# Performance work log

Measured on AMD Instinct MI355X. Metric: run time of the kernel, lower is better.

Reference implementation:

```python
import jax, jax.numpy as jnp
import numpy as np

B, D, NNZ = 64, 8192, 1024      # batch, data_dim, nonzeros per row (exact)
DE, DQK = 256, 256              # id_embed_dim, qk_dim


def setup_inputs() -> dict:
    key = jax.random.key(0)
    k_pos, k_val, k_e, k_wq, k_bq, k_wk, k_bk = jax.random.split(key, 7)
    # x: [B, D] with exactly NNZ nonzero entries per row
    pos = jax.random.uniform(k_pos, (B, D)).argsort(axis=1)[:, :NNZ]  # [B, NNZ]
    vals = jax.random.normal(k_val, (B, NNZ), dtype=jnp.float32)
    vals = jnp.where(vals == 0.0, 1.0, vals)
    x = jnp.zeros((B, D), jnp.float32).at[jnp.arange(B)[:, None], pos].set(vals)
    # parameters (Embedding(D+1, DE), Linear(DE->DQK) x2)
    E = jax.random.normal(k_e, (D + 1, DE), dtype=jnp.float32)
    lim = 1.0 / np.sqrt(DE)
    Wq = jax.random.uniform(k_wq, (DQK, DE), minval=-lim, maxval=lim, dtype=jnp.float32)
    bq = jax.random.uniform(k_bq, (DQK,), minval=-lim, maxval=lim, dtype=jnp.float32)
    Wk = jax.random.uniform(k_wk, (DQK, DE), minval=-lim, maxval=lim, dtype=jnp.float32)
    bk = jax.random.uniform(k_bk, (DQK,), minval=-lim, maxval=lim, dtype=jnp.float32)
    return {"t": 0, "x": x, "E": E, "Wq": Wq, "bq": bq, "Wk": Wk, "bk": bk}


def _condense(x):
    # Vectorized equivalent of the per-row nonzero gather; rows have exactly
    # NNZ nonzeros so max_len == NNZ and positions stay in ascending order
    # (matching torch.nonzero) via a stable sort on the zero-mask.
    mask = (x != 0.0)
    idx = jnp.argsort(jnp.where(mask, 0, 1), axis=1, stable=True)[:, :NNZ]  # [B, NNZ]
    v = jnp.take_along_axis(x, idx, axis=1)                                 # [B, NNZ]
    p = idx + 1                                                             # 1-based ids
    return v, p, idx


def reference(t, x, E, Wq, bq, Wk, bk):
    v, p, idx = _condense(x)                    # [B,L], [B,L]
    e = E[p]                                    # [B,L,DE] embedding gather
    q = jnp.einsum('bld,od->blo', e, Wq) + bq   # [B,L,DQK]
    k = jnp.einsum('bld,od->blo', e, Wk) + bk
    scale = 1.0 / jnp.sqrt(jnp.asarray(DQK, x.dtype))
    S = jnp.einsum('bid,bjd->bij', q, k) * scale  # [B,L,L]
    fx = jnp.einsum('bij,bi->bj', S, v)           # [B,L]
    v_new = v + v * fx
    # decondense: scatter back to dense [B, D]
    y = jnp.zeros_like(x).at[jnp.arange(B)[:, None], idx].set(v_new)
    return y
```

## Files before the change

kernel.cpp:

```cpp
#include <hip/hip_runtime.h>
#include <hip/hip_bf16.h>

constexpr int B   = 64;
constexpr int D   = 8192;
constexpr int NNZ = 1024;
constexpr int DE  = 256;
constexpr int DQK = 256;
constexpr float SCALE = 0.0625f;

constexpr int G     = 16;
constexpr int CHUNK = D / G;

constexpr size_t OFF_MT    = 0;
constexpr size_t OFF_AUX   = 65536;
constexpr size_t OFF_WPART = 66560;
constexpr size_t OFF_SPART = 328704;
constexpr size_t OFF_Z     = 329728;
constexpr size_t OFF_C     = 346112;

__global__ __launch_bounds__(256) void k1_precompute(
    const float* __restrict__ Wq, const float* __restrict__ bq,
    const float* __restrict__ Wk, const float* __restrict__ bk,
    float* __restrict__ ws)
{
    float* MT  = ws + OFF_MT;
    float* aux = ws + OFF_AUX;
    const int blk = blockIdx.x;
    const int tid = threadIdx.x;

    __shared__ float Aq[32][33];
    __shared__ float Bk[32][33];
    __shared__ float sbq[DQK];
    __shared__ float sbk[DQK];
    __shared__ float rp[256];

    if (blk < 64) {
        const int bi = blk >> 3, bj = blk & 7;
        const int I0 = bi * 32, J0 = bj * 32;
        const int lr = tid >> 5;
        const int lc = tid & 31;
        float acc[4] = {0.f, 0.f, 0.f, 0.f};
        for (int oc = 0; oc < DQK; oc += 32) {
            #pragma unroll
            for (int r = 0; r < 4; ++r) {
                int oo = lr + 8 * r;
                Aq[oo][lc] = Wq[(size_t)(oc + oo) * DE + I0 + lc];
                Bk[oo][lc] = Wk[(size_t)(oc + oo) * DE + J0 + lc];
            }
            __syncthreads();
            #pragma unroll
            for (int oo = 0; oo < 32; ++oo) {
                float bv = Bk[oo][lc];
                #pragma unroll
                for (int r = 0; r < 4; ++r)
                    acc[r] += Aq[oo][lr + 8 * r] * bv;
            }
            __syncthreads();
        }
        #pragma unroll
        for (int r = 0; r < 4; ++r)
            MT[(size_t)(I0 + lr + 8 * r) * DE + (J0 + lc)] = acc[r] * SCALE;
    } else {
        sbq[tid] = bq[tid];
        sbk[tid] = bk[tid];
        __syncthreads();
        float a0 = 0.f, a1 = 0.f;
        #pragma unroll 8
        for (int o = 0; o < DQK; ++o) {
            a0 += Wk[(size_t)o * DE + tid] * sbq[o];
            a1 += Wq[(size_t)o * DE + tid] * sbk[o];
        }
        aux[tid]      = a0 * SCALE;
        aux[DE + tid] = a1 * SCALE;
        rp[tid] = sbq[tid] * sbk[tid];
        __syncthreads();
        if (tid < 128) rp[tid] += rp[tid + 128];
        __syncthreads();
        if (tid < 64) {
            float v = rp[tid] + rp[tid + 64];
            for (int off = 32; off; off >>= 1) v += __shfl_xor(v, off);
            if (tid == 0) aux[2 * DE] = v * SCALE;
        }
    }
}

__global__ __launch_bounds__(256) void k2_partial(
    const float* __restrict__ x, const float* __restrict__ E,
    float* __restrict__ ws)
{
    const int blk = blockIdx.x;
    const int b = blk >> 4, g = blk & (G - 1);
    const int tid = threadIdx.x;

    __shared__ int   s_idx[CHUNK];
    __shared__ float s_val[CHUNK];
    __shared__ float s_part[4][DE];
    __shared__ int   s_cnt;
    __shared__ float s_sum;

    if (tid == 0) { s_cnt = 0; s_sum = 0.f; }
    __syncthreads();

    const float* xc = x + (size_t)b * D + (size_t)g * CHUNK;
    float2 v2 = reinterpret_cast<const float2*>(xc)[tid];
    float lsum = 0.f;
    if (v2.x != 0.f) { int pos = atomicAdd(&s_cnt, 1); s_idx[pos] = 2 * tid;     s_val[pos] = v2.x; lsum += v2.x; }
    if (v2.y != 0.f) { int pos = atomicAdd(&s_cnt, 1); s_idx[pos] = 2 * tid + 1; s_val[pos] = v2.y; lsum += v2.y; }
    for (int off = 32; off; off >>= 1) lsum += __shfl_xor(lsum, off);
    if ((tid & 63) == 0) atomicAdd(&s_sum, lsum);
    __syncthreads();

    const int cnt  = s_cnt;
    const int lane = tid & 63;
    const int q    = tid >> 6;
    const int base = g * CHUNK + 1;

    float4 w4 = make_float4(0.f, 0.f, 0.f, 0.f);
    #pragma unroll 2
    for (int j = q; j < cnt; j += 4) {
        int   p = s_idx[j] + base;
        float v = s_val[j];
        float4 e4 = *reinterpret_cast<const float4*>(E + (size_t)p * DE + 4 * lane);
        w4.x += v * e4.x; w4.y += v * e4.y; w4.z += v * e4.z; w4.w += v * e4.w;
    }
    *reinterpret_cast<float4*>(&s_part[q][4 * lane]) = w4;
    __syncthreads();

    float w = s_part[0][tid] + s_part[1][tid] + s_part[2][tid] + s_part[3][tid];
    ws[OFF_WPART + (size_t)blk * DE + tid] = w;
    if (tid == 0) ws[OFF_SPART + blk] = s_sum;
}

__global__ __launch_bounds__(256) void k3_combine(float* __restrict__ ws)
{
    const int b   = blockIdx.x;
    const int tid = threadIdx.x;
    const float* MT  = ws + OFF_MT;
    const float* aux = ws + OFF_AUX;

    __shared__ float s_w[DE];
    __shared__ float rp[256];
    __shared__ float s_s;

    float w = 0.f;
    #pragma unroll
    for (int g = 0; g < G; ++g)
        w += ws[OFF_WPART + ((size_t)(b * G + g)) * DE + tid];
    s_w[tid] = w;

    float s = 0.f;
    if (tid < G) s = ws[OFF_SPART + b * G + tid];
    if (tid < 64) {
        for (int off = 8; off; off >>= 1) s += __shfl_xor(s, off);
        if (tid == 0) s_s = s;
    }
    __syncthreads();

    const float sv = s_s;
    float z0 = 0.f, z1 = 0.f, z2 = 0.f, z3 = 0.f;
    for (int d2 = 0; d2 < DE; d2 += 4) {
        z0 += s_w[d2 + 0] * MT[(size_t)(d2 + 0) * DE + tid];
        z1 += s_w[d2 + 1] * MT[(size_t)(d2 + 1) * DE + tid];
        z2 += s_w[d2 + 2] * MT[(size_t)(d2 + 2) * DE + tid];
        z3 += s_w[d2 + 3] * MT[(size_t)(d2 + 3) * DE + tid];
    }
    float z = (z0 + z1) + (z2 + z3) + sv * aux[tid];
    ws[OFF_Z + (size_t)b * DE + tid] = z;

    rp[tid] = aux[DE + tid] * w;
    __syncthreads();
    if (tid < 128) rp[tid] += rp[tid + 128];
    __syncthreads();
    if (tid < 64) {
        float v = rp[tid] + rp[tid + 64];
        for (int off = 32; off; off >>= 1) v += __shfl_xor(v, off);
        if (tid == 0) ws[OFF_C + b] = v + sv * aux[2 * DE];
    }
}

__global__ __launch_bounds__(256) void k4_scatter(
    const float* __restrict__ x, const float* __restrict__ E,
    const float* __restrict__ ws, float* __restrict__ y)
{
    const int blk = blockIdx.x;
    const int b = blk >> 4, g = blk & (G - 1);
    const int tid = threadIdx.x;

    __shared__ int   s_idx[CHUNK];
    __shared__ float s_val[CHUNK];
    __shared__ float s_z[DE];
    __shared__ int   s_cnt;
    __shared__ float s_c;

    if (tid == 0) { s_cnt = 0; s_c = ws[OFF_C + b]; }
    s_z[tid] = ws[OFF_Z + (size_t)b * DE + tid];
    __syncthreads();

    const float* xc = x + (size_t)b * D + (size_t)g * CHUNK;
    float*       yc = y + (size_t)b * D + (size_t)g * CHUNK;
    float2 v2 = reinterpret_cast<const float2*>(xc)[tid];
    reinterpret_cast<float2*>(yc)[tid] = make_float2(0.f, 0.f);
    if (v2.x != 0.f) { int pos = atomicAdd(&s_cnt, 1); s_idx[pos] = 2 * tid;     s_val[pos] = v2.x; }
    if (v2.y != 0.f) { int pos = atomicAdd(&s_cnt, 1); s_idx[pos] = 2 * tid + 1; s_val[pos] = v2.y; }
    __syncthreads();

    const int cnt  = s_cnt;
    const int lane = tid & 63;
    const int wv   = tid >> 6;
    const int base = g * CHUNK + 1;
    const float c  = s_c;
    float4 z4 = *reinterpret_cast<const float4*>(&s_z[4 * lane]);

    for (int j = wv; j < cnt; j += 4) {
        int p = s_idx[j] + base;
        float4 e4 = *reinterpret_cast<const float4*>(E + (size_t)p * DE + 4 * lane);
        float dot = e4.x * z4.x + e4.y * z4.y + e4.z * z4.z + e4.w * z4.w;
        for (int off = 32; off; off >>= 1) dot += __shfl_xor(dot, off);
        if (lane == 0) yc[s_idx[j]] = s_val[j] * (1.f + dot + c);
    }
}

extern "C" void kernel_launch(void* const* d_in, const int* in_sizes, int n_in,
                              void* d_out, int out_size, void* d_ws, size_t ws_size,
                              hipStream_t stream) {
    const float* x  = (const float*)d_in[1];
    const float* E  = (const float*)d_in[2];
    const float* Wq = (const float*)d_in[3];
    const float* bq = (const float*)d_in[4];
    const float* Wk = (const float*)d_in[5];
    const float* bk = (const float*)d_in[6];
    float* y  = (float*)d_out;
    float* ws = (float*)d_ws;

    hipLaunchKernelGGL(k1_precompute, dim3(65),    dim3(256), 0, stream, Wq, bq, Wk, bk, ws);
    hipLaunchKernelGGL(k2_partial,    dim3(B * G), dim3(256), 0, stream, x, E, ws);
    hipLaunchKernelGGL(k3_combine,    dim3(B),     dim3(256), 0, stream, ws);
    hipLaunchKernelGGL(k4_scatter,    dim3(B * G), dim3(256), 0, stream, x, E, ws, y);
}
```

Before: 108.1 us.

## Fuse precompute with partial pass, cache compacted indices, split combine across columns

Merges the weight-precompute kernel and the partial-sum gather kernel into one launch. The merged kernel also zeroes the output and stores each chunk's compacted nonzero indices and values in the workspace, so the scatter kernel no longer rereads x. The chunk count per row doubles to give more blocks. The combine step now uses four blocks per batch row, each handling a column quarter, to raise parallelism. This removes one launch and one pass over x, at the cost of extra workspace traffic and twice as many partial rows to reduce.

```diff
diff --git a/kernel.cpp b/kernel.cpp
--- a/kernel.cpp
+++ b/kernel.cpp
@@ -8,20 +8,25 @@
 constexpr int DQK = 256;
 constexpr float SCALE = 0.0625f;
 
-constexpr int G     = 16;
+constexpr int G     = 32;
 constexpr int CHUNK = D / G;
+constexpr int NCHUNK = B * G;
 
 constexpr size_t OFF_MT    = 0;
 constexpr size_t OFF_AUX   = 65536;
 constexpr size_t OFF_WPART = 66560;
-constexpr size_t OFF_SPART = 328704;
-constexpr size_t OFF_Z     = 329728;
-constexpr size_t OFF_C     = 346112;
-
-__global__ __launch_bounds__(256) void k1_precompute(
+constexpr size_t OFF_SPART = 590848;
+constexpr size_t OFF_Z     = 592896;
+constexpr size_t OFF_C     = 609280;
+constexpr size_t OFF_CCNT  = 609344;
+constexpr size_t OFF_CIDX  = 611392;
+constexpr size_t OFF_CVAL  = 1135680;
+
+__global__ __launch_bounds__(256) void kA_fused(
+    const float* __restrict__ x, const float* __restrict__ E,
     const float* __restrict__ Wq, const float* __restrict__ bq,
     const float* __restrict__ Wk, const float* __restrict__ bk,
-    float* __restrict__ ws)
+    float* __restrict__ ws, float* __restrict__ y)
 {
     float* MT  = ws + OFF_MT;
     float* aux = ws + OFF_AUX;
@@ -30,9 +35,13 @@
 
     __shared__ float Aq[32][33];
     __shared__ float Bk[32][33];
-    __shared__ float sbq[DQK];
-    __shared__ float sbk[DQK];
-    __shared__ float rp[256];
+    __shared__ float sb0[DQK];
+    __shared__ float sb1[DQK];
+    __shared__ int   s_idx[CHUNK];
+    __shared__ float s_val[CHUNK];
+    __shared__ float s_part[4][DE];
+    __shared__ int   s_cnt;
+    __shared__ float s_sum;
 
     if (blk < 64) {
         const int bi = blk >> 3, bj = blk & 7;
@@ -60,157 +69,160 @@
         #pragma unroll
         for (int r = 0; r < 4; ++r)
             MT[(size_t)(I0 + lr + 8 * r) * DE + (J0 + lc)] = acc[r] * SCALE;
-    } else {
-        sbq[tid] = bq[tid];
-        sbk[tid] = bk[tid];
+    } else if (blk == 64) {
+        sb0[tid] = bq[tid];
+        sb1[tid] = bk[tid];
         __syncthreads();
         float a0 = 0.f, a1 = 0.f;
         #pragma unroll 8
         for (int o = 0; o < DQK; ++o) {
-            a0 += Wk[(size_t)o * DE + tid] * sbq[o];
-            a1 += Wq[(size_t)o * DE + tid] * sbk[o];
+            a0 += Wk[(size_t)o * DE + tid] * sb0[o];
+            a1 += Wq[(size_t)o * DE + tid] * sb1[o];
         }
         aux[tid]      = a0 * SCALE;
         aux[DE + tid] = a1 * SCALE;
-        rp[tid] = sbq[tid] * sbk[tid];
+        s_part[0][tid] = sb0[tid] * sb1[tid];
+        __syncthreads();
+        if (tid < 128) s_part[0][tid] += s_part[0][tid + 128];
+        __syncthreads();
+        if (tid < 64) {
+            float v = s_part[0][tid] + s_part[0][tid + 64];
+            for (int off = 32; off; off >>= 1) v += __shfl_xor(v, off);
+            if (tid == 0) aux[2 * DE] = v * SCALE;
+        }
+    } else {
+        const int cid = blk - 65;
+        const int b = cid >> 5, g = cid & (G - 1);
+        if (tid == 0) { s_cnt = 0; s_sum = 0.f; }
+        __syncthreads();
+
+        const float* xc = x + (size_t)b * D + (size_t)g * CHUNK;
+        float v = xc[tid];
+        y[(size_t)b * D + (size_t)g * CHUNK + tid] = 0.f;
+        float lsum = v;
+        if (v != 0.f) { int pos = atomicAdd(&s_cnt, 1); s_idx[pos] = tid; s_val[pos] = v; }
+        for (int off = 32; off; off >>= 1) lsum += __shfl_xor(lsum, off);
+        if ((tid & 63) == 0) atomicAdd(&s_sum, lsum);
+        __syncthreads();
+
+        const int cnt = s_cnt;
+        if (tid < cnt) {
+            ((int*)(ws + OFF_CIDX))[(size_t)cid * CHUNK + tid] = s_idx[tid];
+            (ws + OFF_CVAL)[(size_t)cid * CHUNK + tid] = s_val[tid];
+        }
+        if (tid == 0) {
+            ((int*)(ws + OFF_CCNT))[cid] = cnt;
+            ws[OFF_SPART + cid] = s_sum;
+        }
+
+        const int lane = tid & 63;
+        const int q    = tid >> 6;
+        const int base = g * CHUNK + 1;
+        float4 w4 = make_float4(0.f, 0.f, 0.f, 0.f);
+        #pragma unroll 2
+        for (int j = q; j < cnt; j += 4) {
+            int   p  = s_idx[j] + base;
+            float vv = s_val[j];
+            float4 e4 = *reinterpret_cast<const float4*>(E + (size_t)p * DE + 4 * lane);
+            w4.x += vv * e4.x; w4.y += vv * e4.y; w4.z += vv * e4.z; w4.w += vv * e4.w;
+        }
+        *reinterpret_cast<float4*>(&s_part[q][4 * lane]) = w4;
+        __syncthreads();
+
+        float w = s_part[0][tid] + s_part[1][tid] + s_part[2][tid] + s_part[3][tid];
+        ws[OFF_WPART + (size_t)cid * DE + tid] = w;
+    }
+}
+
+__global__ __launch_bounds__(256) void kB_combine(float* __restrict__ ws)
+{
+    const int blk = blockIdx.x;
+    const int b = blk >> 2, cg = blk & 3;
+    const int tid = threadIdx.x;
+    const float* MT  = ws + OFF_MT;
+    const float* aux = ws + OFF_AUX;
+
+    __shared__ float s_w[DE];
+    __shared__ float s_mp[4][64];
+    __shared__ float rp[256];
+    __shared__ float s_s;
+
+    float w = 0.f;
+    #pragma unroll 8
+    for (int g = 0; g < G; ++g)
+        w += ws[OFF_WPART + ((size_t)(b * G + g)) * DE + tid];
+    s_w[tid] = w;
+
+    if (tid < 32) {
+        float sv = ws[OFF_SPART + b * G + tid];
+        for (int off = 16; off; off >>= 1) sv += __shfl_xor(sv, off);
+        if (tid == 0) s_s = sv;
+    }
+    __syncthreads();
+
+    const int c = tid & 63, q = tid >> 6;
+    const int ocol = cg * 64 + c;
+    float acc = 0.f;
+    #pragma unroll 8
+    for (int d2 = q * 64; d2 < q * 64 + 64; ++d2)
+        acc += s_w[d2] * MT[(size_t)d2 * DE + ocol];
+    s_mp[q][c] = acc;
+    __syncthreads();
+
+    if (tid < 64) {
+        float z = s_mp[0][tid] + s_mp[1][tid] + s_mp[2][tid] + s_mp[3][tid]
+                + s_s * aux[cg * 64 + tid];
+        ws[OFF_Z + (size_t)b * DE + cg * 64 + tid] = z;
+    }
+
+    if (cg == 0) {
+        rp[tid] = aux[DE + tid] * s_w[tid];
         __syncthreads();
         if (tid < 128) rp[tid] += rp[tid + 128];
         __syncthreads();
         if (tid < 64) {
             float v = rp[tid] + rp[tid + 64];
             for (int off = 32; off; off >>= 1) v += __shfl_xor(v, off);
-            if (tid == 0) aux[2 * DE] = v * SCALE;
-        }
-    }
-}
-
-__global__ __launch_bounds__(256) void k2_partial(
-    const float* __restrict__ x, const float* __restrict__ E,
-    float* __restrict__ ws)
+            if (tid == 0) ws[OFF_C + b] = v + s_s * aux[2 * DE];
+        }
+    }
+}
+
+__global__ __launch_bounds__(256, 8) void kC_scatter(
+    const float* __restrict__ E, const float* __restrict__ ws,
+    float* __restrict__ y)
 {
-    const int blk = blockIdx.x;
-    const int b = blk >> 4, g = blk & (G - 1);
-    const int tid = threadIdx.x;
-
-    __shared__ int   s_idx[CHUNK];
-    __shared__ float s_val[CHUNK];
-    __shared__ float s_part[4][DE];
-    __shared__ int   s_cnt;
-    __shared__ float s_sum;
-
-    if (tid == 0) { s_cnt = 0; s_sum = 0.f; }
-    __syncthreads();
-
-    const float* xc = x + (size_t)b * D + (size_t)g * CHUNK;
-    float2 v2 = reinterpret_cast<const float2*>(xc)[tid];
-    float lsum = 0.f;
-    if (v2.x != 0.f) { int pos = atomicAdd(&s_cnt, 1); s_idx[pos] = 2 * tid;     s_val[pos] = v2.x; lsum += v2.x; }
-    if (v2.y != 0.f) { int pos = atomicAdd(&s_cnt, 1); s_idx[pos] = 2 * tid + 1; s_val[pos] = v2.y; lsum += v2.y; }
-    for (int off = 32; off; off >>= 1) lsum += __shfl_xor(lsum, off);
-    if ((tid & 63) == 0) atomicAdd(&s_sum, lsum);
-    __syncthreads();
-
-    const int cnt  = s_cnt;
-    const int lane = tid & 63;
-    const int q    = tid >> 6;
-    const int base = g * CHUNK + 1;
-
-    float4 w4 = make_float4(0.f, 0.f, 0.f, 0.f);
-    #pragma unroll 2
-    for (int j = q; j < cnt; j += 4) {
-        int   p = s_idx[j] + base;
-        float v = s_val[j];
-        float4 e4 = *reinterpret_cast<const float4*>(E + (size_t)p * DE + 4 * lane);
-        w4.x += v * e4.x; w4.y += v * e4.y; w4.z += v * e4.z; w4.w += v * e4.w;
-    }
-    *reinterpret_cast<float4*>(&s_part[q][4 * lane]) = w4;
-    __syncthreads();
-
-    float w = s_part[0][tid] + s_part[1][tid] + s_part[2][tid] + s_part[3][tid];
-    ws[OFF_WPART + (size_t)blk * DE + tid] = w;
-    if (tid == 0) ws[OFF_SPART + blk] = s_sum;
-}
-
-__global__ __launch_bounds__(256) void k3_combine(float* __restrict__ ws)
-{
-    const int b   = blockIdx.x;
-    const int tid = threadIdx.x;
-    const float* MT  = ws + OFF_MT;
-    const float* aux = ws + OFF_AUX;
-
-    __shared__ float s_w[DE];
-    __shared__ float rp[256];
-    __shared__ float s_s;
-
-    float w = 0.f;
-    #pragma unroll
-    for (int g = 0; g < G; ++g)
-        w += ws[OFF_WPART + ((size_t)(b * G + g)) * DE + tid];
-    s_w[tid] = w;
-
-    float s = 0.f;
-    if (tid < G) s = ws[OFF_SPART + b * G + tid];
-    if (tid < 64) {
-        for (int off = 8; off; off >>= 1) s += __shfl_xor(s, off);
-        if (tid == 0) s_s = s;
-    }
-    __syncthreads();
-
-    const float sv = s_s;
-    float z0 = 0.f, z1 = 0.f, z2 = 0.f, z3 = 0.f;
-    for (int d2 = 0; d2 < DE; d2 += 4) {
-        z0 += s_w[d2 + 0] * MT[(size_t)(d2 + 0) * DE + tid];
-        z1 += s_w[d2 + 1] * MT[(size_t)(d2 + 1) * DE + tid];
-        z2 += s_w[d2 + 2] * MT[(size_t)(d2 + 2) * DE + tid];
-        z3 += s_w[d2 + 3] * MT[(size_t)(d2 + 3) * DE + tid];
-    }
-    float z = (z0 + z1) + (z2 + z3) + sv * aux[tid];
-    ws[OFF_Z + (size_t)b * DE + tid] = z;
-
-    rp[tid] = aux[DE + tid] * w;
-    __syncthreads();
-    if (tid < 128) rp[tid] += rp[tid + 128];
-    __syncthreads();
-    if (tid < 64) {
-        float v = rp[tid] + rp[tid + 64];
-        for (int off = 32; off; off >>= 1) v += __shfl_xor(v, off);
-        if (tid == 0) ws[OFF_C + b] = v + sv * aux[2 * DE];
-    }
-}
-
-__global__ __launch_bounds__(256) void k4_scatter(
-    const float* __restrict__ x, const float* __restrict__ E,
-    const float* __restrict__ ws, float* __restrict__ y)
-{
-    const int blk = blockIdx.x;
-    const int b = blk >> 4, g = blk & (G - 1);
+    const int cid = blockIdx.x;
+    const int b = cid >> 5, g = cid & (G - 1);
     const int tid = threadIdx.x;
 
     __shared__ int   s_idx[CHUNK];
     __shared__ float s_val[CHUNK];
     __shared__ float s_z[DE];
-    __shared__ int   s_cnt;
     __shared__ float s_c;
-
-    if (tid == 0) { s_cnt = 0; s_c = ws[OFF_C + b]; }
+    __shared__ int   s_n;
+
     s_z[tid] = ws[OFF_Z + (size_t)b * DE + tid];
-    __syncthreads();
-
-    const float* xc = x + (size_t)b * D + (size_t)g * CHUNK;
-    float*       yc = y + (size_t)b * D + (size_t)g * CHUNK;
-    float2 v2 = reinterpret_cast<const float2*>(xc)[tid];
-    reinterpret_cast<float2*>(yc)[tid] = make_float2(0.f, 0.f);
-    if (v2.x != 0.f) { int pos = atomicAdd(&s_cnt, 1); s_idx[pos] = 2 * tid;     s_val[pos] = v2.x; }
-    if (v2.y != 0.f) { int pos = atomicAdd(&s_cnt, 1); s_idx[pos] = 2 * tid + 1; s_val[pos] = v2.y; }
-    __syncthreads();
-
-    const int cnt  = s_cnt;
+    if (tid == 0) {
+        s_c = ws[OFF_C + b];
+        s_n = ((const int*)(ws + OFF_CCNT))[cid];
+    }
+    __syncthreads();
+    const int cnt = s_n;
+    if (tid < cnt) {
+        s_idx[tid] = ((const int*)(ws + OFF_CIDX))[(size_t)cid * CHUNK + tid];
+        s_val[tid] = (ws + OFF_CVAL)[(size_t)cid * CHUNK + tid];
+    }
+    __syncthreads();
+
     const int lane = tid & 63;
     const int wv   = tid >> 6;
     const int base = g * CHUNK + 1;
     const float c  = s_c;
     float4 z4 = *reinterpret_cast<const float4*>(&s_z[4 * lane]);
-
+    float* yc = y + (size_t)b * D + (size_t)g * CHUNK;
+
+    #pragma unroll 2
     for (int j = wv; j < cnt; j += 4) {
         int p = s_idx[j] + base;
         float4 e4 = *reinterpret_cast<const float4*>(E + (size_t)p * DE + 4 * lane);
@@ -232,8 +244,8 @@
     float* y  = (float*)d_out;
     float* ws = (float*)d_ws;
 
-    hipLaunchKernelGGL(k1_precompute, dim3(65),    dim3(256), 0, stream, Wq, bq, Wk, bk, ws);
-    hipLaunchKernelGGL(k2_partial,    dim3(B * G), dim3(256), 0, stream, x, E, ws);
-    hipLaunchKernelGGL(k3_combine,    dim3(B),     dim3(256), 0, stream, ws);
-    hipLaunchKernelGGL(k4_scatter,    dim3(B * G), dim3(256), 0, stream, x, E, ws, y);
-}
+    hipLaunchKernelGGL(kA_fused,   dim3(65 + NCHUNK), dim3(256), 0, stream,
+                       x, E, Wq, bq, Wk, bk, ws, y);
+    hipLaunchKernelGGL(kB_combine, dim3(B * 4),       dim3(256), 0, stream, ws);
+    hipLaunchKernelGGL(kC_scatter, dim3(NCHUNK),      dim3(256), 0, stream, E, ws, y);
+}
```

Measured after the change: 102.3 us. -5.3%, faster.

## Replace sparse gather with dense tiled GEMMs over x and E, fuse precompute

Applied to the files above, without the earlier changes.

Drops the per-row nonzero compaction and instead treats x as dense. W = x·E[1:] is computed as a tiled GEMM split over D chunks, and y = x ⊙ (1 + E·Z + c) as a second tiled GEMM whose epilogue reads x directly. The Wq/Wk precompute is folded into the first kernel's grid, cutting launches from four to three. This trades irregular gathered E-row loads, shuffle reductions and scattered writes for coalesced, reuse-friendly loads, at the cost of doing dense work over all D entries (8x more FLOPs than the nonzeros need) and a larger partial-sum workspace.

```diff
diff --git a/kernel.cpp b/kernel.cpp
--- a/kernel.cpp
+++ b/kernel.cpp
@@ -3,39 +3,80 @@
 
 constexpr int B   = 64;
 constexpr int D   = 8192;
-constexpr int NNZ = 1024;
 constexpr int DE  = 256;
 constexpr int DQK = 256;
 constexpr float SCALE = 0.0625f;
 
-constexpr int G     = 16;
-constexpr int CHUNK = D / G;
+constexpr int NKC = 64;
+constexpr int KD  = D / NKC;
 
 constexpr size_t OFF_MT    = 0;
 constexpr size_t OFF_AUX   = 65536;
-constexpr size_t OFF_WPART = 66560;
-constexpr size_t OFF_SPART = 328704;
-constexpr size_t OFF_Z     = 329728;
-constexpr size_t OFF_C     = 346112;
-
-__global__ __launch_bounds__(256) void k1_precompute(
+constexpr size_t OFF_WPART = 66112;
+constexpr size_t OFF_Z     = 1114688;
+constexpr size_t OFF_C     = 1131072;
+
+__global__ __launch_bounds__(256, 2) void kA(
+    const float* __restrict__ x, const float* __restrict__ E,
     const float* __restrict__ Wq, const float* __restrict__ bq,
     const float* __restrict__ Wk, const float* __restrict__ bk,
     float* __restrict__ ws)
 {
-    float* MT  = ws + OFF_MT;
-    float* aux = ws + OFF_AUX;
+    __shared__ __align__(16) char smem[68608];
     const int blk = blockIdx.x;
     const int tid = threadIdx.x;
 
-    __shared__ float Aq[32][33];
-    __shared__ float Bk[32][33];
-    __shared__ float sbq[DQK];
-    __shared__ float sbk[DQK];
-    __shared__ float rp[256];
-
-    if (blk < 64) {
-        const int bi = blk >> 3, bj = blk & 7;
+    if (blk < 256) {
+        const int kc  = blk >> 2;
+        const int tqb = blk & 3;
+        float (*Xl)[132] = (float(*)[132])smem;
+        float (*Et)[68]  = (float(*)[68])(smem + 33792);
+
+        #pragma unroll
+        for (int i = 0; i < 8; ++i) {
+            int f4 = i * 256 + tid;
+            int r = f4 >> 5, c4 = f4 & 31;
+            float4 v = *reinterpret_cast<const float4*>(
+                x + (size_t)r * D + kc * KD + 4 * c4);
+            *reinterpret_cast<float4*>(&Xl[r][4 * c4]) = v;
+        }
+        #pragma unroll
+        for (int i = 0; i < 8; ++i) {
+            int f4 = i * 256 + tid;
+            int r = f4 >> 4, c4 = f4 & 15;
+            float4 v = *reinterpret_cast<const float4*>(
+                E + (size_t)(kc * KD + r + 1) * DE + tqb * 64 + 4 * c4);
+            *reinterpret_cast<float4*>(&Et[r][4 * c4]) = v;
+        }
+        __syncthreads();
+
+        const int bq4 = tid >> 4;
+        const int tq4 = tid & 15;
+        float acc[4][4] = {};
+        #pragma unroll 4
+        for (int k = 0; k < KD; ++k) {
+            const float e0 = Et[k][4 * tq4 + 0];
+            const float e1 = Et[k][4 * tq4 + 1];
+            const float e2 = Et[k][4 * tq4 + 2];
+            const float e3 = Et[k][4 * tq4 + 3];
+            #pragma unroll
+            for (int i = 0; i < 4; ++i) {
+                const float xv = Xl[4 * bq4 + i][k];
+                acc[i][0] += xv * e0; acc[i][1] += xv * e1;
+                acc[i][2] += xv * e2; acc[i][3] += xv * e3;
+            }
+        }
+        float* WP = ws + OFF_WPART + (size_t)kc * (64 * 256);
+        #pragma unroll
+        for (int i = 0; i < 4; ++i)
+            *reinterpret_cast<float4*>(
+                WP + (size_t)(4 * bq4 + i) * 256 + tqb * 64 + 4 * tq4) =
+                make_float4(acc[i][0], acc[i][1], acc[i][2], acc[i][3]);
+    } else if (blk < 320) {
+        const int mb = blk - 256;
+        float (*Aq)[33] = (float(*)[33])smem;
+        float (*Bk)[33] = (float(*)[33])(smem + 4224);
+        const int bi = mb >> 3, bj = mb & 7;
         const int I0 = bi * 32, J0 = bj * 32;
         const int lr = tid >> 5;
         const int lc = tid & 31;
@@ -57,166 +98,155 @@
             }
             __syncthreads();
         }
+        float* MT = ws + OFF_MT;
         #pragma unroll
         for (int r = 0; r < 4; ++r)
             MT[(size_t)(I0 + lr + 8 * r) * DE + (J0 + lc)] = acc[r] * SCALE;
     } else {
-        sbq[tid] = bq[tid];
-        sbk[tid] = bk[tid];
+        float* sb0 = (float*)smem;
+        float* sb1 = sb0 + 256;
+        float* rp  = sb1 + 256;
+        float* aux = ws + OFF_AUX;
+        sb0[tid] = bq[tid];
+        sb1[tid] = bk[tid];
         __syncthreads();
         float a0 = 0.f, a1 = 0.f;
         #pragma unroll 8
         for (int o = 0; o < DQK; ++o) {
-            a0 += Wk[(size_t)o * DE + tid] * sbq[o];
-            a1 += Wq[(size_t)o * DE + tid] * sbk[o];
-        }
-        aux[tid]      = a0 * SCALE;
-        aux[DE + tid] = a1 * SCALE;
-        rp[tid] = sbq[tid] * sbk[tid];
+            a0 += Wk[(size_t)o * DE + tid] * sb0[o];
+            a1 += Wq[(size_t)o * DE + tid] * sb1[o];
+        }
+        aux[tid]       = a0 * SCALE;
+        aux[256 + tid] = a1 * SCALE;
+        rp[tid] = sb0[tid] * sb1[tid];
         __syncthreads();
         if (tid < 128) rp[tid] += rp[tid + 128];
         __syncthreads();
         if (tid < 64) {
             float v = rp[tid] + rp[tid + 64];
             for (int off = 32; off; off >>= 1) v += __shfl_xor(v, off);
-            if (tid == 0) aux[2 * DE] = v * SCALE;
-        }
-    }
-}
-
-__global__ __launch_bounds__(256) void k2_partial(
-    const float* __restrict__ x, const float* __restrict__ E,
-    float* __restrict__ ws)
-{
-    const int blk = blockIdx.x;
-    const int b = blk >> 4, g = blk & (G - 1);
-    const int tid = threadIdx.x;
-
-    __shared__ int   s_idx[CHUNK];
-    __shared__ float s_val[CHUNK];
-    __shared__ float s_part[4][DE];
-    __shared__ int   s_cnt;
-    __shared__ float s_sum;
-
-    if (tid == 0) { s_cnt = 0; s_sum = 0.f; }
-    __syncthreads();
-
-    const float* xc = x + (size_t)b * D + (size_t)g * CHUNK;
-    float2 v2 = reinterpret_cast<const float2*>(xc)[tid];
-    float lsum = 0.f;
-    if (v2.x != 0.f) { int pos = atomicAdd(&s_cnt, 1); s_idx[pos] = 2 * tid;     s_val[pos] = v2.x; lsum += v2.x; }
-    if (v2.y != 0.f) { int pos = atomicAdd(&s_cnt, 1); s_idx[pos] = 2 * tid + 1; s_val[pos] = v2.y; lsum += v2.y; }
-    for (int off = 32; off; off >>= 1) lsum += __shfl_xor(lsum, off);
-    if ((tid & 63) == 0) atomicAdd(&s_sum, lsum);
-    __syncthreads();
-
-    const int cnt  = s_cnt;
-    const int lane = tid & 63;
-    const int q    = tid >> 6;
-    const int base = g * CHUNK + 1;
-
-    float4 w4 = make_float4(0.f, 0.f, 0.f, 0.f);
-    #pragma unroll 2
-    for (int j = q; j < cnt; j += 4) {
-        int   p = s_idx[j] + base;
-        float v = s_val[j];
-        float4 e4 = *reinterpret_cast<const float4*>(E + (size_t)p * DE + 4 * lane);
-        w4.x += v * e4.x; w4.y += v * e4.y; w4.z += v * e4.z; w4.w += v * e4.w;
-    }
-    *reinterpret_cast<float4*>(&s_part[q][4 * lane]) = w4;
-    __syncthreads();
-
-    float w = s_part[0][tid] + s_part[1][tid] + s_part[2][tid] + s_part[3][tid];
-    ws[OFF_WPART + (size_t)blk * DE + tid] = w;
-    if (tid == 0) ws[OFF_SPART + blk] = s_sum;
-}
-
-__global__ __launch_bounds__(256) void k3_combine(float* __restrict__ ws)
+            if (tid == 0) aux[512] = v * SCALE;
+        }
+    }
+}
+
+__global__ __launch_bounds__(256) void kB(
+    const float* __restrict__ x, float* __restrict__ ws)
 {
     const int b   = blockIdx.x;
     const int tid = threadIdx.x;
-    const float* MT  = ws + OFF_MT;
-    const float* aux = ws + OFF_AUX;
-
-    __shared__ float s_w[DE];
-    __shared__ float rp[256];
+    __shared__ float wl[256];
+    __shared__ float red[256];
     __shared__ float s_s;
 
+    float ps = 0.f;
+    const float4* xr = reinterpret_cast<const float4*>(x + (size_t)b * D);
+    #pragma unroll 8
+    for (int i = tid; i < D / 4; i += 256) {
+        float4 v = xr[i];
+        ps += (v.x + v.y) + (v.z + v.w);
+    }
+    red[tid] = ps;
+
     float w = 0.f;
-    #pragma unroll
-    for (int g = 0; g < G; ++g)
-        w += ws[OFF_WPART + ((size_t)(b * G + g)) * DE + tid];
-    s_w[tid] = w;
-
-    float s = 0.f;
-    if (tid < G) s = ws[OFF_SPART + b * G + tid];
+    #pragma unroll 8
+    for (int kc = 0; kc < NKC; ++kc)
+        w += ws[OFF_WPART + (size_t)kc * (64 * 256) + (size_t)b * 256 + tid];
+    wl[tid] = w;
+    __syncthreads();
+
+    if (tid < 128) red[tid] += red[tid + 128];
+    __syncthreads();
     if (tid < 64) {
-        for (int off = 8; off; off >>= 1) s += __shfl_xor(s, off);
-        if (tid == 0) s_s = s;
-    }
-    __syncthreads();
-
+        float v = red[tid] + red[tid + 64];
+        for (int off = 32; off; off >>= 1) v += __shfl_xor(v, off);
+        if (tid == 0) s_s = v;
+    }
+    __syncthreads();
     const float sv = s_s;
-    float z0 = 0.f, z1 = 0.f, z2 = 0.f, z3 = 0.f;
-    for (int d2 = 0; d2 < DE; d2 += 4) {
-        z0 += s_w[d2 + 0] * MT[(size_t)(d2 + 0) * DE + tid];
-        z1 += s_w[d2 + 1] * MT[(size_t)(d2 + 1) * DE + tid];
-        z2 += s_w[d2 + 2] * MT[(size_t)(d2 + 2) * DE + tid];
-        z3 += s_w[d2 + 3] * MT[(size_t)(d2 + 3) * DE + tid];
-    }
-    float z = (z0 + z1) + (z2 + z3) + sv * aux[tid];
-    ws[OFF_Z + (size_t)b * DE + tid] = z;
-
-    rp[tid] = aux[DE + tid] * w;
-    __syncthreads();
-    if (tid < 128) rp[tid] += rp[tid + 128];
+
+    float z = sv * ws[OFF_AUX + tid];
+    #pragma unroll 8
+    for (int d2 = 0; d2 < 256; ++d2)
+        z += wl[d2] * ws[OFF_MT + (size_t)d2 * 256 + tid];
+    ws[OFF_Z + (size_t)tid * B + b] = z;
+
+    red[tid] = ws[OFF_AUX + 256 + tid] * w;
+    __syncthreads();
+    if (tid < 128) red[tid] += red[tid + 128];
     __syncthreads();
     if (tid < 64) {
-        float v = rp[tid] + rp[tid + 64];
+        float v = red[tid] + red[tid + 64];
         for (int off = 32; off; off >>= 1) v += __shfl_xor(v, off);
-        if (tid == 0) ws[OFF_C + b] = v + sv * aux[2 * DE];
-    }
-}
-
-__global__ __launch_bounds__(256) void k4_scatter(
+        if (tid == 0) ws[OFF_C + b] = v + sv * ws[OFF_AUX + 512];
+    }
+}
+
+__global__ __launch_bounds__(256, 2) void kC(
     const float* __restrict__ x, const float* __restrict__ E,
     const float* __restrict__ ws, float* __restrict__ y)
 {
-    const int blk = blockIdx.x;
-    const int b = blk >> 4, g = blk & (G - 1);
+    const int d0  = blockIdx.x * 32;
     const int tid = threadIdx.x;
 
-    __shared__ int   s_idx[CHUNK];
-    __shared__ float s_val[CHUNK];
-    __shared__ float s_z[DE];
-    __shared__ int   s_cnt;
-    __shared__ float s_c;
-
-    if (tid == 0) { s_cnt = 0; s_c = ws[OFF_C + b]; }
-    s_z[tid] = ws[OFF_Z + (size_t)b * DE + tid];
-    __syncthreads();
-
-    const float* xc = x + (size_t)b * D + (size_t)g * CHUNK;
-    float*       yc = y + (size_t)b * D + (size_t)g * CHUNK;
-    float2 v2 = reinterpret_cast<const float2*>(xc)[tid];
-    reinterpret_cast<float2*>(yc)[tid] = make_float2(0.f, 0.f);
-    if (v2.x != 0.f) { int pos = atomicAdd(&s_cnt, 1); s_idx[pos] = 2 * tid;     s_val[pos] = v2.x; }
-    if (v2.y != 0.f) { int pos = atomicAdd(&s_cnt, 1); s_idx[pos] = 2 * tid + 1; s_val[pos] = v2.y; }
-    __syncthreads();
-
-    const int cnt  = s_cnt;
-    const int lane = tid & 63;
-    const int wv   = tid >> 6;
-    const int base = g * CHUNK + 1;
-    const float c  = s_c;
-    float4 z4 = *reinterpret_cast<const float4*>(&s_z[4 * lane]);
-
-    for (int j = wv; j < cnt; j += 4) {
-        int p = s_idx[j] + base;
-        float4 e4 = *reinterpret_cast<const float4*>(E + (size_t)p * DE + 4 * lane);
-        float dot = e4.x * z4.x + e4.y * z4.y + e4.z * z4.z + e4.w * z4.w;
-        for (int off = 32; off; off >>= 1) dot += __shfl_xor(dot, off);
-        if (lane == 0) yc[s_idx[j]] = s_val[j] * (1.f + dot + c);
+    __shared__ float Zl[256][64];
+    __shared__ float Et[32][68];
+
+    #pragma unroll
+    for (int i = 0; i < 64; ++i)
+        (&Zl[0][0])[i * 256 + tid] = ws[OFF_Z + (size_t)i * 256 + tid];
+    __syncthreads();
+
+    const int dq  = tid >> 4;
+    const int bq4 = tid & 15;
+    float acc[2][4] = {};
+
+    for (int ks = 0; ks < 4; ++ks) {
+        #pragma unroll
+        for (int i = 0; i < 2; ++i) {
+            int f4 = i * 256 + tid;
+            int r = f4 >> 4, c4 = f4 & 15;
+            float4 v = *reinterpret_cast<const float4*>(
+                E + (size_t)(d0 + r + 1) * DE + ks * 64 + 4 * c4);
+            *reinterpret_cast<float4*>(&Et[r][4 * c4]) = v;
+        }
+        __syncthreads();
+        #pragma unroll 4
+        for (int tt = 0; tt < 64; ++tt) {
+            const float4 z4 = *reinterpret_cast<const float4*>(
+                &Zl[ks * 64 + tt][4 * bq4]);
+            const float e0 = Et[2 * dq + 0][tt];
+            const float e1 = Et[2 * dq + 1][tt];
+            acc[0][0] += e0 * z4.x; acc[0][1] += e0 * z4.y;
+            acc[0][2] += e0 * z4.z; acc[0][3] += e0 * z4.w;
+            acc[1][0] += e1 * z4.x; acc[1][1] += e1 * z4.y;
+            acc[1][2] += e1 * z4.z; acc[1][3] += e1 * z4.w;
+        }
+        __syncthreads();
+    }
+
+    #pragma unroll
+    for (int i = 0; i < 2; ++i)
+        *reinterpret_cast<float4*>(&Et[2 * dq + i][4 * bq4]) =
+            make_float4(acc[i][0], acc[i][1], acc[i][2], acc[i][3]);
+    __syncthreads();
+
+    {
+        const int b  = tid >> 2;
+        const int ds = (tid & 3) * 8;
+        const float cc = ws[OFF_C + b];
+        const float* xr = x + (size_t)b * D + d0 + ds;
+        float*       yr = y + (size_t)b * D + d0 + ds;
+        #pragma unroll
+        for (int k4 = 0; k4 < 2; ++k4) {
+            float4 xv = *reinterpret_cast<const float4*>(xr + 4 * k4);
+            float4 yv;
+            yv.x = xv.x * (1.f + Et[ds + 4 * k4 + 0][b] + cc);
+            yv.y = xv.y * (1.f + Et[ds + 4 * k4 + 1][b] + cc);
+            yv.z = xv.z * (1.f + Et[ds + 4 * k4 + 2][b] + cc);
+            yv.w = xv.w * (1.f + Et[ds + 4 * k4 + 3][b] + cc);
+            *reinterpret_cast<float4*>(yr + 4 * k4) = yv;
+        }
     }
 }
 
@@ -232,8 +262,7 @@
     float* y  = (float*)d_out;
     float* ws = (float*)d_ws;
 
-    hipLaunchKernelGGL(k1_precompute, dim3(65),    dim3(256), 0, stream, Wq, bq, Wk, bk, ws);
-    hipLaunchKernelGGL(k2_partial,    dim3(B * G), dim3(256), 0, stream, x, E, ws);
-    hipLaunchKernelGGL(k3_combine,    dim3(B),     dim3(256), 0, stream, ws);
-    hipLaunchKernelGGL(k4_scatter,    dim3(B * G), dim3(256), 0, stream, x, E, ws, y);
-}
+    hipLaunchKernelGGL(kA, dim3(321), dim3(256), 0, stream, x, E, Wq, bq, Wk, bk, ws);
+    hipLaunchKernelGGL(kB, dim3(B),   dim3(256), 0, stream, x, ws);
+    hipLaunchKernelGGL(kC, dim3(256), dim3(256), 0, stream, x, E, ws, y);
+}
```

New measurement: 115.6 us. 7.0% more time.
